# Optimization experiments

Measured on AMD Instinct MI355X. Metric: run time of the kernel, lower is better.

The kernel has to match this reference:

```python
import jax, jax.numpy as jnp
import numpy as np

B, I, H = 16384, 1024, 1024
LN_EPS = 1e-5


def setup_inputs() -> dict:
    key = jax.random.key(0)
    k1, k2, k3, k4 = jax.random.split(key, 4)
    x = jax.random.normal(k1, (B, I), dtype=jnp.float32)
    h_out = jax.random.normal(k2, (B, H), dtype=jnp.float32)
    cell = jax.random.normal(k3, (B, H), dtype=jnp.float32)
    # nn.Linear(i_size + h, 4*h, bias=False): weight shape [4h, i+h]
    W = jax.random.normal(k4, (4 * H, I + H), dtype=jnp.float32) * (1.0 / np.sqrt(I + H))
    gamma = jnp.ones((4, H), dtype=jnp.float32)
    beta = jnp.zeros((4, H), dtype=jnp.float32)
    return {"x": x, "h_out": h_out, "cell": cell, "W": W, "gamma": gamma, "beta": beta}


def reference(x, h_out, cell, W, gamma, beta):
    # concat + linear -> [B, 4, H]
    cat = jnp.concatenate([x, h_out], axis=-1)               # [B, I+H]
    t = (cat @ W.T).reshape(cat.shape[0], 4, H)              # [B, 4, H]
    # LayerNorm over normalized_shape=(4, H): stats over last two dims
    mu = jnp.mean(t, axis=(-2, -1), keepdims=True)
    var = jnp.mean(jnp.square(t - mu), axis=(-2, -1), keepdims=True)
    handle = (t - mu) * jax.lax.rsqrt(var + LN_EPS) * gamma + beta
    # gates: first 3 slices sigmoid, last slice GELU (exact, eval-mode dropout = identity)
    gates = jax.nn.sigmoid(handle[:, 0:3, :])
    f_gate, i_gate, o_gate = gates[:, 0], gates[:, 1], gates[:, 2]
    h_cand = jax.nn.gelu(handle[:, 3, :], approximate=False)
    new_cell = f_gate * cell + i_gate * h_cand
    new_out = o_gate * new_cell
    return (new_out, new_cell)
```

## Files before the change

### kernel.cpp

```cpp
#include <hip/hip_runtime.h>
#include <stdint.h>

#define B_ROWS 16384
#define IN_DIM 1024
#define H_DIM  1024
#define KDIM   2048
#define NDIM   4096
#define LN_EPSF 1e-5f

typedef unsigned short u16;
typedef float  f32x4  __attribute__((ext_vector_type(4)));
typedef float  fv4    __attribute__((ext_vector_type(4)));
typedef __bf16 bf16x8 __attribute__((ext_vector_type(8)));
typedef u16    u16x4  __attribute__((ext_vector_type(4)));
typedef u16    u16x8  __attribute__((ext_vector_type(8)));

__device__ __forceinline__ u16 f2bf(float f) {
  unsigned u = __float_as_uint(f);
  u += 0x7FFFu + ((u >> 16) & 1u);
  return (u16)(u >> 16);
}
__device__ __forceinline__ float bf2f(u16 s) {
  return __uint_as_float(((unsigned)s) << 16);
}

#define GLOAD_LDS16(gp, lp) __builtin_amdgcn_global_load_lds( \
    (__attribute__((address_space(1))) void*)(gp),            \
    (__attribute__((address_space(3))) void*)(lp), 16, 0, 0)

__global__ __launch_bounds__(256) void cast_concat(
    const float* __restrict__ x, const float* __restrict__ h,
    u16* __restrict__ cat) {
  int idx = blockIdx.x * 256 + threadIdx.x;
  long base = (long)idx * 8;
  int  c = (int)(base & (KDIM - 1));
  long b = base >> 11;
  const float* src = (c < IN_DIM) ? (x + b * IN_DIM + c)
                                  : (h + b * H_DIM + (c - IN_DIM));
  fv4 v0 = *(const fv4*)(src);
  fv4 v1 = *(const fv4*)(src + 4);
  u16x8 o;
  o[0]=f2bf(v0[0]); o[1]=f2bf(v0[1]); o[2]=f2bf(v0[2]); o[3]=f2bf(v0[3]);
  o[4]=f2bf(v1[0]); o[5]=f2bf(v1[1]); o[6]=f2bf(v1[2]); o[7]=f2bf(v1[3]);
  *(u16x8*)(cat + base) = o;
}

__global__ __launch_bounds__(256) void cast_plain(
    const float* __restrict__ w, u16* __restrict__ wb) {
  int idx = blockIdx.x * 256 + threadIdx.x;
  long base = (long)idx * 8;
  fv4 v0 = *(const fv4*)(w + base);
  fv4 v1 = *(const fv4*)(w + base + 4);
  u16x8 o;
  o[0]=f2bf(v0[0]); o[1]=f2bf(v0[1]); o[2]=f2bf(v0[2]); o[3]=f2bf(v0[3]);
  o[4]=f2bf(v1[0]); o[5]=f2bf(v1[1]); o[6]=f2bf(v1[2]); o[7]=f2bf(v1[3]);
  *(u16x8*)(wb + base) = o;
}


#define STA(S_, P_, T_) GLOAD_LDS16(pA + (size_t)(P_) * 64 * KDIM + (T_) * 64, \
                                    &LA[S_][(P_) * 4096 + tid * 8])
#define STB(S_, P_, T_) GLOAD_LDS16(pB + (size_t)(P_) * 64 * KDIM + (T_) * 64, \
                                    &LB[S_][(P_) * 4096 + tid * 8])

#define RDA(S_, MB_) { const u16* ap = &LA[S_][abase + ((MB_) >> 2) * 4096];  \
  _Pragma("unroll") for (int i_ = 0; i_ < 4; ++i_) {                          \
    a[i_][0] = *(const bf16x8*)(ap + i_ * 1024 + kk0);                        \
    a[i_][1] = *(const bf16x8*)(ap + i_ * 1024 + kk1); } }

#define RDB(S_, V_, NB_) { const u16* bp = &LB[S_][bbase + (NB_) * 1024];     \
  _Pragma("unroll") for (int i_ = 0; i_ < 2; ++i_) {                          \
    V_[i_][0] = *(const bf16x8*)(bp + i_ * 1024 + kk0);                       \
    V_[i_][1] = *(const bf16x8*)(bp + i_ * 1024 + kk1); } }

#define MQ(MB_, NB_, V_)                                                      \
  _Pragma("unroll") for (int m_ = 0; m_ < 4; ++m_)                            \
  _Pragma("unroll") for (int n_ = 0; n_ < 2; ++n_) {                          \
    acc[(MB_) + m_][(NB_) + n_] = __builtin_amdgcn_mfma_f32_16x16x32_bf16(    \
        a[m_][0], V_[n_][0], acc[(MB_) + m_][(NB_) + n_], 0, 0, 0);           \
    acc[(MB_) + m_][(NB_) + n_] = __builtin_amdgcn_mfma_f32_16x16x32_bf16(    \
        a[m_][1], V_[n_][1], acc[(MB_) + m_][(NB_) + n_], 0, 0, 0); }

#define HEAD                                                                  \
  __builtin_amdgcn_sched_barrier(0);                                          \
  __builtin_amdgcn_s_barrier();                                               \
  asm volatile("s_waitcnt lgkmcnt(0)" ::: "memory");                          \
  __builtin_amdgcn_sched_barrier(0);                                          \
  __builtin_amdgcn_s_setprio(1);

#define TAIL                                                                  \
  __builtin_amdgcn_s_setprio(0);                                              \
  __builtin_amdgcn_sched_barrier(0);                                          \
  __builtin_amdgcn_s_barrier();

__global__ __launch_bounds__(512, 2) void gemm_bt(
    const u16* __restrict__ A,
    const u16* __restrict__ Bw,
    u16* __restrict__ C) {
  __shared__ u16 LA[2][16384];
  __shared__ u16 LB[2][16384];

  const int tid  = threadIdx.x;
  const int lane = tid & 63;
  const int wave = tid >> 6;
  const int wm   = wave >> 2;
  const int wn   = wave & 3;
  const int r    = lane & 15;
  const int g    = lane >> 4;

  const int bid = blockIdx.x;
  const int xcd = bid & 7;
  const int k_  = bid >> 3;
  const int row0 = (xcd * 8 + (k_ >> 4)) * 256;
  const int col0 = (k_ & 15) * 256;

  const int l    = tid ^ ((tid >> 3) & 7);
  const int srow = l >> 3;
  const int skc  = (l & 7) * 8;
  const u16* pA = A  + (size_t)(row0 + srow) * KDIM + skc;
  const u16* pB = Bw + (size_t)(col0 + srow) * KDIM + skc;

  const int rx   = r & 7;
  const int kk0  = ((g      ) ^ rx) << 3;
  const int kk1  = (((4 | g)) ^ rx) << 3;
  const int abase = wm * 8192 + r * 64;
  const int bbase = wn * 4096 + r * 64;

  f32x4 acc[8][4] = {};
  bf16x8 a[4][2], b0[2][2], b1[2][2];

  STA(0, 0, 0); STA(0, 1, 0); STA(0, 2, 0); STA(0, 3, 0);
  STB(0, 0, 0); STB(0, 1, 0); STB(0, 2, 0); STB(0, 3, 0);
  STA(1, 0, 1); STA(1, 2, 1);
  STB(1, 0, 1); STB(1, 1, 1); STB(1, 2, 1); STB(1, 3, 1);
  asm volatile("s_waitcnt vmcnt(6)" ::: "memory");
  __builtin_amdgcn_s_barrier();

  for (int it = 0; it < 16; ++it) {
    const int u = 2 * it;
    const bool st = it < 15;

    RDA(0, 0); RDB(0, b0, 0);
    STA(1, 1, u + 1); STA(1, 3, u + 1);
    asm volatile("s_waitcnt lgkmcnt(8)" ::: "memory");
    HEAD; MQ(0, 0, b0); TAIL;

    RDB(0, b1, 2);
    if (st) { STA(0, 0, u + 2); STA(0, 2, u + 2); }
    HEAD; MQ(0, 2, b1); TAIL;

    RDA(0, 4);
    if (st) { STB(0, 0, u + 2); STB(0, 1, u + 2); }
    HEAD; MQ(4, 0, b0); TAIL;

    if (st) { STB(0, 2, u + 2); STB(0, 3, u + 2); }
    HEAD; MQ(4, 2, b1);
    __builtin_amdgcn_s_setprio(0);
    __builtin_amdgcn_sched_barrier(0);
    if (st) { asm volatile("s_waitcnt vmcnt(4)" ::: "memory"); }
    else    { asm volatile("s_waitcnt vmcnt(0)" ::: "memory"); }
    __builtin_amdgcn_s_barrier();

    RDA(1, 0); RDB(1, b0, 0);
    if (st) { STA(0, 1, u + 2); STA(0, 3, u + 2); }
    asm volatile("s_waitcnt lgkmcnt(8)" ::: "memory");
    HEAD; MQ(0, 0, b0); TAIL;

    RDB(1, b1, 2);
    if (st) { STA(1, 0, u + 3); STA(1, 2, u + 3); }
    HEAD; MQ(0, 2, b1); TAIL;

    RDA(1, 4);
    if (st) { STB(1, 0, u + 3); STB(1, 1, u + 3); }
    HEAD; MQ(4, 0, b0); TAIL;

    if (st) { STB(1, 2, u + 3); STB(1, 3, u + 3); }
    HEAD; MQ(4, 2, b1);
    __builtin_amdgcn_s_setprio(0);
    __builtin_amdgcn_sched_barrier(0);
    if (st) { asm volatile("s_waitcnt vmcnt(6)" ::: "memory"); }
    __builtin_amdgcn_s_barrier();
  }

#pragma unroll
  for (int m = 0; m < 8; ++m)
#pragma unroll
    for (int n = 0; n < 4; ++n)
#pragma unroll
      for (int q = 0; q < 4; ++q) {
        const int rr = row0 + wm * 128 + m * 16 + g * 4 + q;
        const int cc = col0 + wn * 64 + n * 16 + r;
        C[(size_t)rr * NDIM + cc] = f2bf(acc[m][n][q]);
      }
}

__global__ __launch_bounds__(256) void ln_gates(
    const u16* __restrict__ t,
    const float* __restrict__ cell,
    const float* __restrict__ gamma,
    const float* __restrict__ beta,
    float* __restrict__ out) {
  const int b   = blockIdx.x;
  const int tid = threadIdx.x;
  const int h0  = tid * 4;

  const u16* trow = t + (long)b * NDIM;
  float v[4][4];
#pragma unroll
  for (int gi = 0; gi < 4; ++gi) {
    u16x4 raw = *(const u16x4*)&trow[gi * H_DIM + h0];
#pragma unroll
    for (int j = 0; j < 4; ++j) v[gi][j] = bf2f(raw[j]);
  }

  float s1 = 0.f, s2 = 0.f;
#pragma unroll
  for (int gi = 0; gi < 4; ++gi)
#pragma unroll
    for (int j = 0; j < 4; ++j) { s1 += v[gi][j]; s2 += v[gi][j] * v[gi][j]; }

#pragma unroll
  for (int m = 32; m; m >>= 1) {
    s1 += __shfl_xor(s1, m);
    s2 += __shfl_xor(s2, m);
  }
  __shared__ float red[2][4];
  const int wave = tid >> 6, lane = tid & 63;
  if (lane == 0) { red[0][wave] = s1; red[1][wave] = s2; }
  __syncthreads();
  s1 = red[0][0] + red[0][1] + red[0][2] + red[0][3];
  s2 = red[1][0] + red[1][1] + red[1][2] + red[1][3];

  const float mean  = s1 * (1.f / (float)NDIM);
  const float var   = s2 * (1.f / (float)NDIM) - mean * mean;
  const float scale = rsqrtf(var + LN_EPSF);

  float hd[4][4];
#pragma unroll
  for (int gi = 0; gi < 4; ++gi) {
    fv4 gm = *(const fv4*)&gamma[gi * H_DIM + h0];
    fv4 bt = *(const fv4*)&beta[gi * H_DIM + h0];
#pragma unroll
    for (int j = 0; j < 4; ++j)
      hd[gi][j] = (v[gi][j] - mean) * scale * gm[j] + bt[j];
  }

  fv4 cv = *(const fv4*)&cell[(long)b * H_DIM + h0];
  fv4 no, nc;
#pragma unroll
  for (int j = 0; j < 4; ++j) {
    float fg = 1.f / (1.f + expf(-hd[0][j]));
    float ig = 1.f / (1.f + expf(-hd[1][j]));
    float og = 1.f / (1.f + expf(-hd[2][j]));
    float hc = 0.5f * hd[3][j] * (1.f + erff(hd[3][j] * 0.70710678118654752f));
    float ncell = fg * cv[j] + ig * hc;
    nc[j] = ncell;
    no[j] = og * ncell;
  }
  *(fv4*)&out[(long)b * H_DIM + h0] = no;
  *(fv4*)&out[(long)B_ROWS * H_DIM + (long)b * H_DIM + h0] = nc;
}

extern "C" void kernel_launch(void* const* d_in, const int* in_sizes, int n_in,
                              void* d_out, int out_size, void* d_ws, size_t ws_size,
                              hipStream_t stream) {
  const float* x     = (const float*)d_in[0];
  const float* h     = (const float*)d_in[1];
  const float* cell  = (const float*)d_in[2];
  const float* W     = (const float*)d_in[3];
  const float* gamma = (const float*)d_in[4];
  const float* beta  = (const float*)d_in[5];
  float* out = (float*)d_out;

  const size_t cat_bytes = (size_t)B_ROWS * KDIM * sizeof(u16);
  const size_t w_bytes   = (size_t)NDIM * KDIM * sizeof(u16);
  const size_t t_bytes   = (size_t)B_ROWS * NDIM * sizeof(u16);
  if (ws_size < cat_bytes + w_bytes + t_bytes) return;

  uint8_t* ws = (uint8_t*)d_ws;
  u16* catb = (u16*)ws;
  u16* Wb   = (u16*)(ws + cat_bytes);
  u16* tbuf = (u16*)(ws + cat_bytes + w_bytes);

  cast_concat<<<(B_ROWS * (long)KDIM / 8) / 256, 256, 0, stream>>>(x, h, catb);
  cast_plain<<<(NDIM * (long)KDIM / 8) / 256, 256, 0, stream>>>(W, Wb);

  gemm_bt<<<dim3(1024), 512, 0, stream>>>(catb, Wb, tbuf);

  ln_gates<<<B_ROWS, 256, 0, stream>>>(tbuf, cell, gamma, beta, out);
}
```

Before: 364.7 us.

## Double-buffer LDS fragment registers to prefetch across GEMM phases

Restructures the bf16 GEMM main loop so A and B fragments are read from LDS into alternating register sets (aP/aQ, bP/bQ) one phase ahead of the MFMA block that uses them. Each phase now waits only on its own LDS reads via partial lgkmcnt instead of draining all of them, and the global-to-LDS prefetch schedule is reordered to match. The goal is to hide LDS read latency behind MFMA work, at the cost of more registers and a more fragile hand-tuned waitcnt and barrier schedule.

```diff
diff --git a/kernel.cpp b/kernel.cpp
--- a/kernel.cpp
+++ b/kernel.cpp
@@ -63,32 +63,30 @@
 #define STB(S_, P_, T_) GLOAD_LDS16(pB + (size_t)(P_) * 64 * KDIM + (T_) * 64, \
                                     &LB[S_][(P_) * 4096 + tid * 8])
 
-#define RDA(S_, MB_) { const u16* ap = &LA[S_][abase + ((MB_) >> 2) * 4096];  \
+#define RDA(S_, D_, MB_) { const u16* ap_ = &LA[S_][abase + ((MB_) >> 2) * 4096]; \
   _Pragma("unroll") for (int i_ = 0; i_ < 4; ++i_) {                          \
-    a[i_][0] = *(const bf16x8*)(ap + i_ * 1024 + kk0);                        \
-    a[i_][1] = *(const bf16x8*)(ap + i_ * 1024 + kk1); } }
-
-#define RDB(S_, V_, NB_) { const u16* bp = &LB[S_][bbase + (NB_) * 1024];     \
+    D_[i_][0] = *(const bf16x8*)(ap_ + i_ * 1024 + kk0);                      \
+    D_[i_][1] = *(const bf16x8*)(ap_ + i_ * 1024 + kk1); } }
+
+#define RDB(S_, D_, NB_) { const u16* bp_ = &LB[S_][bbase + (NB_) * 1024];    \
   _Pragma("unroll") for (int i_ = 0; i_ < 2; ++i_) {                          \
-    V_[i_][0] = *(const bf16x8*)(bp + i_ * 1024 + kk0);                       \
-    V_[i_][1] = *(const bf16x8*)(bp + i_ * 1024 + kk1); } }
-
-#define MQ(MB_, NB_, V_)                                                      \
+    D_[i_][0] = *(const bf16x8*)(bp_ + i_ * 1024 + kk0);                      \
+    D_[i_][1] = *(const bf16x8*)(bp_ + i_ * 1024 + kk1); } }
+
+#define MQ(MB_, A_, NB_, B_)                                                  \
   _Pragma("unroll") for (int m_ = 0; m_ < 4; ++m_)                            \
   _Pragma("unroll") for (int n_ = 0; n_ < 2; ++n_) {                          \
     acc[(MB_) + m_][(NB_) + n_] = __builtin_amdgcn_mfma_f32_16x16x32_bf16(    \
-        a[m_][0], V_[n_][0], acc[(MB_) + m_][(NB_) + n_], 0, 0, 0);           \
+        A_[m_][0], B_[n_][0], acc[(MB_) + m_][(NB_) + n_], 0, 0, 0);          \
     acc[(MB_) + m_][(NB_) + n_] = __builtin_amdgcn_mfma_f32_16x16x32_bf16(    \
-        a[m_][1], V_[n_][1], acc[(MB_) + m_][(NB_) + n_], 0, 0, 0); }
-
-#define HEAD                                                                  \
-  __builtin_amdgcn_sched_barrier(0);                                          \
-  __builtin_amdgcn_s_barrier();                                               \
-  asm volatile("s_waitcnt lgkmcnt(0)" ::: "memory");                          \
+        A_[m_][1], B_[n_][1], acc[(MB_) + m_][(NB_) + n_], 0, 0, 0); }
+
+#define PHW(N_)                                                               \
+  asm volatile("s_waitcnt lgkmcnt(" #N_ ")" ::: "memory");                    \
   __builtin_amdgcn_sched_barrier(0);                                          \
   __builtin_amdgcn_s_setprio(1);
 
-#define TAIL                                                                  \
+#define PHE                                                                   \
   __builtin_amdgcn_s_setprio(0);                                              \
   __builtin_amdgcn_sched_barrier(0);                                          \
   __builtin_amdgcn_s_barrier();
@@ -121,65 +119,78 @@
   const u16* pB = Bw + (size_t)(col0 + srow) * KDIM + skc;
 
   const int rx   = r & 7;
-  const int kk0  = ((g      ) ^ rx) << 3;
-  const int kk1  = (((4 | g)) ^ rx) << 3;
+  const int kk0  = ((g    ) ^ rx) << 3;
+  const int kk1  = ((4 | g) ^ rx) << 3;
   const int abase = wm * 8192 + r * 64;
   const int bbase = wn * 4096 + r * 64;
 
   f32x4 acc[8][4] = {};
-  bf16x8 a[4][2], b0[2][2], b1[2][2];
-
-  STA(0, 0, 0); STA(0, 1, 0); STA(0, 2, 0); STA(0, 3, 0);
-  STB(0, 0, 0); STB(0, 1, 0); STB(0, 2, 0); STB(0, 3, 0);
-  STA(1, 0, 1); STA(1, 2, 1);
-  STB(1, 0, 1); STB(1, 1, 1); STB(1, 2, 1); STB(1, 3, 1);
-  asm volatile("s_waitcnt vmcnt(6)" ::: "memory");
+  bf16x8 aP[4][2], aQ[4][2], bP[2][2], bQ[2][2];
+
+  STA(0, 0, 0); STA(0, 2, 0); STB(0, 0, 0); STB(0, 1, 0);
+  STB(0, 2, 0); STB(0, 3, 0); STA(0, 1, 0); STA(0, 3, 0);
+  STA(1, 0, 1); STA(1, 2, 1); STB(1, 0, 1); STB(1, 1, 1);
+  STB(1, 2, 1); STB(1, 3, 1); STA(1, 1, 1); STA(1, 3, 1);
+  asm volatile("s_waitcnt vmcnt(8)" ::: "memory");
   __builtin_amdgcn_s_barrier();
+  RDA(0, aP, 0);
+  RDB(0, bP, 0);
 
   for (int it = 0; it < 16; ++it) {
     const int u = 2 * it;
     const bool st = it < 15;
 
-    RDA(0, 0); RDB(0, b0, 0);
-    STA(1, 1, u + 1); STA(1, 3, u + 1);
-    asm volatile("s_waitcnt lgkmcnt(8)" ::: "memory");
-    HEAD; MQ(0, 0, b0); TAIL;
-
-    RDB(0, b1, 2);
+    RDB(0, bQ, 2);
     if (st) { STA(0, 0, u + 2); STA(0, 2, u + 2); }
-    HEAD; MQ(0, 2, b1); TAIL;
-
-    RDA(0, 4);
+    PHW(4); MQ(0, aP, 0, bP); PHE;
+
+    RDA(0, aQ, 4);
     if (st) { STB(0, 0, u + 2); STB(0, 1, u + 2); }
-    HEAD; MQ(4, 0, b0); TAIL;
-
-    if (st) { STB(0, 2, u + 2); STB(0, 3, u + 2); }
-    HEAD; MQ(4, 2, b1);
+    PHW(8); MQ(0, aP, 2, bQ);
     __builtin_amdgcn_s_setprio(0);
     __builtin_amdgcn_sched_barrier(0);
     if (st) { asm volatile("s_waitcnt vmcnt(4)" ::: "memory"); }
     else    { asm volatile("s_waitcnt vmcnt(0)" ::: "memory"); }
     __builtin_amdgcn_s_barrier();
 
-    RDA(1, 0); RDB(1, b0, 0);
+    RDA(1, aP, 0);
+    if (st) { STB(0, 2, u + 2); STB(0, 3, u + 2); }
+    PHW(8); MQ(4, aQ, 0, bP); PHE;
+
+    RDB(1, bP, 0);
     if (st) { STA(0, 1, u + 2); STA(0, 3, u + 2); }
-    asm volatile("s_waitcnt lgkmcnt(8)" ::: "memory");
-    HEAD; MQ(0, 0, b0); TAIL;
-
-    RDB(1, b1, 2);
+    PHW(4); MQ(4, aQ, 2, bQ); PHE;
+
+    RDB(1, bQ, 2);
     if (st) { STA(1, 0, u + 3); STA(1, 2, u + 3); }
-    HEAD; MQ(0, 2, b1); TAIL;
-
-    RDA(1, 4);
+    PHW(4); MQ(0, aP, 0, bP); PHE;
+
+    RDA(1, aQ, 4);
     if (st) { STB(1, 0, u + 3); STB(1, 1, u + 3); }
-    HEAD; MQ(4, 0, b0); TAIL;
-
-    if (st) { STB(1, 2, u + 3); STB(1, 3, u + 3); }
-    HEAD; MQ(4, 2, b1);
+    PHW(8); MQ(0, aP, 2, bQ);
     __builtin_amdgcn_s_setprio(0);
     __builtin_amdgcn_sched_barrier(0);
-    if (st) { asm volatile("s_waitcnt vmcnt(6)" ::: "memory"); }
+    if (st) { asm volatile("s_waitcnt vmcnt(4)" ::: "memory"); }
+    else    { asm volatile("s_waitcnt vmcnt(0)" ::: "memory"); }
     __builtin_amdgcn_s_barrier();
+
+    if (st) {
+      RDA(0, aP, 0);
+      STB(1, 2, u + 3); STB(1, 3, u + 3);
+      PHW(8);
+    } else {
+      PHW(0);
+    }
+    MQ(4, aQ, 0, bP); PHE;
+
+    if (st) {
+      RDB(0, bP, 0);
+      STA(1, 1, u + 3); STA(1, 3, u + 3);
+      PHW(4);
+    } else {
+      PHW(0);
+    }
+    MQ(4, aQ, 2, bQ); PHE;
   }
 
 #pragma unroll
```

Measured after the change: 389.3 us. 6.7% more time.
